# Kernel tuning notes

Measured on AMD Instinct MI355X. Metric: run time of the kernel, lower is better.

The kernel has to match this reference:

```python
import jax, jax.numpy as jnp
import numpy as np

N_NODES = 100000
N_EDGES = 1600000
D_IN = 128
D_HID = 128
D_OUT = 128


def setup_inputs() -> dict:
    key = jax.random.key(0)
    ks = jax.random.split(key, 12)
    x = jax.random.normal(ks[0], (N_NODES, D_IN), dtype=jnp.float32)
    edge_index = jax.random.randint(ks[1], (2, N_EDGES), 0, N_NODES, dtype=jnp.int64)
    s = 0.05
    # GraphConv layer l: out = agg @ w_rel + x @ w_root + b  (lin_rel has bias, lin_root does not)
    w_rel1 = jax.random.normal(ks[2], (D_IN, D_HID), dtype=jnp.float32) * s
    w_root1 = jax.random.normal(ks[3], (D_IN, D_HID), dtype=jnp.float32) * s
    b1 = jax.random.normal(ks[4], (D_HID,), dtype=jnp.float32) * s
    w_rel2 = jax.random.normal(ks[5], (D_HID, D_HID), dtype=jnp.float32) * s
    w_root2 = jax.random.normal(ks[6], (D_HID, D_HID), dtype=jnp.float32) * s
    b2 = jax.random.normal(ks[7], (D_HID,), dtype=jnp.float32) * s
    w_rel3 = jax.random.normal(ks[8], (D_HID, D_OUT), dtype=jnp.float32) * s
    w_root3 = jax.random.normal(ks[9], (D_HID, D_OUT), dtype=jnp.float32) * s
    b3 = jax.random.normal(ks[10], (D_OUT,), dtype=jnp.float32) * s
    return {"x": x, "edge_index": edge_index,
            "w_rel1": w_rel1, "w_root1": w_root1, "b1": b1,
            "w_rel2": w_rel2, "w_root2": w_root2, "b2": b2,
            "w_rel3": w_rel3, "w_root3": w_root3, "b3": b3}


def _graph_conv(h, src, dst, w_rel, w_root, b):
    # sum-aggregate neighbor features (message = x_j, flow src -> dst),
    # then linear; identical math to PyG GraphConv with aggr='add'.
    agg = jax.ops.segment_sum(h[src], dst, num_segments=h.shape[0])
    return agg @ w_rel + h @ w_root + b


def reference(x, edge_index, w_rel1, w_root1, b1, w_rel2, w_root2, b2, w_rel3, w_root3, b3):
    src, dst = edge_index[0], edge_index[1]
    h = jax.nn.relu(_graph_conv(x, src, dst, w_rel1, w_root1, b1))
    h = jax.nn.relu(_graph_conv(h, src, dst, w_rel2, w_root2, b2))
    out = _graph_conv(h, src, dst, w_rel3, w_root3, b3)
    return out
```

## Files before the change

### kernel.cpp

```cpp
#include <hip/hip_runtime.h>
#include <hip/hip_bf16.h>
#include <stdint.h>

typedef __hip_bfloat16 bf16;
typedef __hip_bfloat162 bf162;

typedef __attribute__((ext_vector_type(8))) short short8;
typedef __attribute__((ext_vector_type(4))) float floatx4;

#define BSH   8
#define BSZ   256
#define CHUNK 8192
#define NBMAX 512
#define NSLAB 8



__device__ __forceinline__ void acc2(float& a, float& b, unsigned u) {
    a += __uint_as_float(u << 16);
    b += __uint_as_float(u & 0xffff0000u);
}

__global__ __launch_bounds__(256)
void prep_bhist_kernel(const float* __restrict__ x, bf16* __restrict__ y, int n4, int nCvt,
                       const float* __restrict__ wr1, const float* __restrict__ wo1,
                       const float* __restrict__ wr2, const float* __restrict__ wo2,
                       const float* __restrict__ wr3, const float* __restrict__ wo3,
                       bf16* __restrict__ w1, bf16* __restrict__ w2, bf16* __restrict__ w3,
                       const int* __restrict__ dst, int* __restrict__ T,
                       int E, int NB, int GB) {
    __shared__ int lh[NBMAX];
    const int b = blockIdx.x;
    if (b < nCvt) {
        const int i = b * 256 + threadIdx.x;
        if (i < n4) {
            const int N = n4 >> 5;
            const int n = i >> 5;
            const int q = i & 31;
            float4 v = ((const float4*)x)[i];
            union { bf16 bb[4]; unsigned long long u; } pk;
            pk.bb[0] = __float2bfloat16(v.x);
            pk.bb[1] = __float2bfloat16(v.y);
            pk.bb[2] = __float2bfloat16(v.z);
            pk.bb[3] = __float2bfloat16(v.w);
            *(unsigned long long*)(y + ((size_t)(q >> 2) * N + n) * 16 + (q & 3) * 4) = pk.u;
        }
        return;
    }
    if (b < nCvt + 48) {
        int t = (b - nCvt) * 256 + threadIdx.x;
        const int layer = t >> 12;
        t &= 4095;
        const float* wrel  = (layer == 0) ? wr1 : (layer == 1) ? wr2 : wr3;
        const float* wroot = (layer == 0) ? wo1 : (layer == 1) ? wo2 : wo3;
        bf16*        wsw   = (layer == 0) ? w1  : (layer == 1) ? w2  : w3;
        const int lane = t & 63;
        const int ct   = (t >> 6) & 7;
        const int kt   = t >> 9;
        const int kbase = kt * 32 + (lane >> 4) * 8;
        const int n     = ct * 16 + (lane & 15);
        bf16* q = wsw + (size_t)t * 8;
#pragma unroll
        for (int j = 0; j < 8; ++j) {
            const int k = kbase + j;
            const float v = (k < 128) ? wrel[k * 128 + n] : wroot[(k - 128) * 128 + n];
            q[j] = __float2bfloat16(v);
        }
        return;
    }
    const int bb = b - nCvt - 48;
    for (int u = threadIdx.x; u < NB; u += 256) lh[u] = 0;
    __syncthreads();
    const int beg = bb * CHUNK, end = min(beg + CHUNK, E);
    for (int e = beg + threadIdx.x; e < end; e += 256)
        atomicAdd(&lh[dst[e] >> BSH], 1);
    __syncthreads();
    for (int u = threadIdx.x; u < NB; u += 256)
        T[u * GB + bb] = lh[u];
}


__global__ __launch_bounds__(256)
void scan1_kernel(const int* __restrict__ deg, int* __restrict__ rp,
                  int* __restrict__ bsum, int n) {
    __shared__ int s[256];
    const int tid = threadIdx.x;
    const int i = blockIdx.x * 256 + tid;
    const int d = (i < n) ? deg[i] : 0;
    s[tid] = d;
    __syncthreads();
    for (int off = 1; off < 256; off <<= 1) {
        int u = (tid >= off) ? s[tid - off] : 0;
        __syncthreads();
        s[tid] += u;
        __syncthreads();
    }
    if (i < n) rp[i] = s[tid] - d;
    if (tid == 255) bsum[blockIdx.x] = s[255];
}

__global__ __launch_bounds__(512)
void scan2_kernel(int* __restrict__ bsum, int G) {
    __shared__ int s[512];
    const int tid = threadIdx.x;
    const int d = (tid < G) ? bsum[tid] : 0;
    s[tid] = d;
    __syncthreads();
    for (int off = 1; off < 512; off <<= 1) {
        int u = (tid >= off) ? s[tid - off] : 0;
        __syncthreads();
        s[tid] += u;
        __syncthreads();
    }
    if (tid < G) bsum[tid] = s[tid] - d;
}


__global__ __launch_bounds__(256)
void bscatter_kernel(const int* __restrict__ src, const int* __restrict__ dst,
                     const int* __restrict__ T, const int* __restrict__ bsum,
                     int* __restrict__ ebuf, int E, int NB, int GB) {
    __shared__ int lofs[NBMAX];
    const int b = blockIdx.x;
    for (int u = threadIdx.x; u < NB; u += 256) {
        const int idx = u * GB + b;
        lofs[u] = T[idx] + bsum[idx >> 8];
    }
    __syncthreads();
    const int beg = b * CHUNK, end = min(beg + CHUNK, E);
    for (int e = beg + threadIdx.x; e < end; e += 256) {
        const int d = dst[e];
        const int u = d >> BSH;
        const int pos = atomicAdd(&lofs[u], 1);
        ebuf[pos] = (src[e] << BSH) | (d & (BSZ - 1));
    }
}

__global__ __launch_bounds__(256)
void bbuild_kernel(const int* __restrict__ T, const int* __restrict__ bsum,
                   const int* __restrict__ ebuf,
                   int* __restrict__ rp, int* __restrict__ col,
                   int E, int N, int NB, int GB) {
    __shared__ int s[256];
    __shared__ int lrank[256];
    const int u = blockIdx.x;
    const int tid = threadIdx.x;
    const int i0 = u * GB;
    const int beg = T[i0] + bsum[i0 >> 8];
    const int i1 = (u + 1) * GB;
    const int end = (u + 1 < NB) ? (T[i1] + bsum[i1 >> 8]) : E;

    lrank[tid] = 0;
    __syncthreads();
    for (int e = beg + tid; e < end; e += 256)
        atomicAdd(&lrank[ebuf[e] & (BSZ - 1)], 1);
    __syncthreads();
    const int cntv = lrank[tid];
    s[tid] = cntv;
    __syncthreads();
    for (int off = 1; off < 256; off <<= 1) {
        int v = (tid >= off) ? s[tid - off] : 0;
        __syncthreads();
        s[tid] += v;
        __syncthreads();
    }
    const int excl = s[tid] - cntv;
    const int node = u * BSZ + tid;
    if (node < N) rp[node] = beg + excl;
    if (u == NB - 1 && tid == 0) rp[N] = E;
    lrank[tid] = beg + excl;
    __syncthreads();
    for (int e = beg + tid; e < end; e += 256) {
        const int p = ebuf[e];
        const int pos = atomicAdd(&lrank[p & (BSZ - 1)], 1);
        col[pos] = p >> BSH;
    }
}


__global__ __launch_bounds__(512)
void agg_kernel(const bf16* __restrict__ h, const int* __restrict__ rp,
                const int* __restrict__ col, bf16* __restrict__ agg, int N) {
    const int s    = blockIdx.x & 7;
    const int tid  = threadIdx.x;
    const int wid  = tid >> 6;
    const int lane = tid & 63;
    const int g    = lane >> 2;
    const int fl   = lane & 3;
    const int node = (blockIdx.x >> 3) * 128 + wid * 16 + g;
    if (node >= N) return;

    const bf16* Hs = h + (size_t)s * N * 16;
    const int beg = rp[node], end = rp[node + 1];

    float a0 = 0.f, a1 = 0.f, a2 = 0.f, a3 = 0.f;
    int e = beg;
#pragma unroll 2
    for (; e + 2 <= end; e += 2) {
        const int s0 = col[e];
        const int s1 = col[e + 1];
        const uint2 r0 = *(const uint2*)(Hs + (size_t)s0 * 16 + fl * 4);
        const uint2 r1 = *(const uint2*)(Hs + (size_t)s1 * 16 + fl * 4);
        acc2(a0, a1, r0.x); acc2(a2, a3, r0.y);
        acc2(a0, a1, r1.x); acc2(a2, a3, r1.y);
    }
    if (e < end) {
        const int s0 = col[e];
        const uint2 r0 = *(const uint2*)(Hs + (size_t)s0 * 16 + fl * 4);
        acc2(a0, a1, r0.x); acc2(a2, a3, r0.y);
    }

    union { bf16 bb[4]; unsigned long long u; } pk;
    pk.bb[0] = __float2bfloat16(a0);
    pk.bb[1] = __float2bfloat16(a1);
    pk.bb[2] = __float2bfloat16(a2);
    pk.bb[3] = __float2bfloat16(a3);
    __builtin_nontemporal_store(pk.u,
        (unsigned long long*)(agg + ((size_t)s * N + node) * 16 + fl * 4));
}


template <bool RELU, typename OT>
__global__ __launch_bounds__(512)
void mfma_gemm_kernel(const bf16* __restrict__ Aagg, const bf16* __restrict__ Hroot,
                      const bf16* __restrict__ wsw, const float* __restrict__ bias,
                      OT* __restrict__ out, int M) {
    __shared__ __align__(16) char smem[67584];
    const int tid = threadIdx.x;

#pragma unroll
    for (int i = 0; i < 8; ++i) {
        const int off = i * 8192 + tid * 16;
        *(float4*)(smem + off) = *(const float4*)((const char*)wsw + off);
    }
    __syncthreads();

    const int lane = tid & 63;
    const int wave = tid >> 6;
    const int l15  = lane & 15;
    const int quad = lane >> 4;
    const int base = blockIdx.x * 128;
    const int row_a = base + wave * 16 + l15;
    const bool rowok = row_a < M;
    const bf16* wl = (const bf16*)smem;

    floatx4 acc[8];
#pragma unroll
    for (int ct = 0; ct < 8; ++ct) acc[ct] = (floatx4){0.f, 0.f, 0.f, 0.f};

#pragma unroll
    for (int kt = 0; kt < 8; ++kt) {
        const bf16* Abase = (kt < 4) ? Aagg : Hroot;
        const int k0 = (kt & 3) * 32 + quad * 8;
        short8 afrag = (short8){0, 0, 0, 0, 0, 0, 0, 0};
        if (rowok)
            afrag = *(const short8*)(Abase + ((size_t)(k0 >> 4) * M + row_a) * 16 + (k0 & 15));
#pragma unroll
        for (int ct = 0; ct < 8; ++ct) {
            const short8 bfrag = *(const short8*)(wl + (size_t)((kt * 8 + ct) * 64 + lane) * 8);
            acc[ct] = __builtin_amdgcn_mfma_f32_16x16x32_bf16(afrag, bfrag, acc[ct], 0, 0, 0);
        }
    }

    __syncthreads();
    const int rloc = wave * 16 + quad * 4;

    if constexpr (sizeof(OT) == 2) {
        bf16* tl = (bf16*)smem;
#pragma unroll
        for (int ct = 0; ct < 8; ++ct) {
            const int colc = ct * 16 + l15;
            const float bv = bias[colc];
#pragma unroll
            for (int r = 0; r < 4; ++r) {
                float v = acc[ct][r] + bv;
                if (RELU) v = fmaxf(v, 0.f);
                tl[(rloc + r) * 136 + colc] = __float2bfloat16(v);
            }
        }
        __syncthreads();
#pragma unroll
        for (int i = 0; i < 4; ++i) {
            const int chunk = i * 512 + tid;
            const int slab = chunk >> 8;
            const int r    = (chunk >> 1) & 127;
            const int half = chunk & 1;
            if (base + r < M)
                *(float4*)((char*)out + ((size_t)slab * M + base + r) * 32 + half * 16) =
                    *(const float4*)(smem + r * 272 + slab * 32 + half * 16);
        }
    } else {
        float* tl = (float*)smem;
#pragma unroll
        for (int ct = 0; ct < 8; ++ct) {
            const int colc = ct * 16 + l15;
            const float bv = bias[colc];
#pragma unroll
            for (int r = 0; r < 4; ++r) {
                float v = acc[ct][r] + bv;
                if (RELU) v = fmaxf(v, 0.f);
                tl[(rloc + r) * 132 + colc] = v;
            }
        }
        __syncthreads();
#pragma unroll
        for (int i = 0; i < 8; ++i) {
            const int chunk = i * 512 + tid;
            const int row = chunk >> 5;
            const int c   = chunk & 31;
            if (base + row < M)
                *(float4*)((char*)out + (size_t)(base + row) * 512 + c * 16) =
                    *(const float4*)(smem + row * 528 + c * 16);
        }
    }
}


extern "C" void kernel_launch(void* const* d_in, const int* in_sizes, int n_in,
                              void* d_out, int out_size, void* d_ws, size_t ws_size,
                              hipStream_t stream) {
    const float* x       = (const float*)d_in[0];
    const int*   ei      = (const int*)d_in[1];
    const float* w_rel1  = (const float*)d_in[2];
    const float* w_root1 = (const float*)d_in[3];
    const float* b1      = (const float*)d_in[4];
    const float* w_rel2  = (const float*)d_in[5];
    const float* w_root2 = (const float*)d_in[6];
    const float* b2      = (const float*)d_in[7];
    const float* w_rel3  = (const float*)d_in[8];
    const float* w_root3 = (const float*)d_in[9];
    const float* b3      = (const float*)d_in[10];
    float* out = (float*)d_out;

    const int N = in_sizes[0] / 128;
    const int E = in_sizes[1] / 2;
    const int* src = ei;
    const int* dst = ei + E;

    char* w = (char*)d_ws;
    auto alloc = [&](size_t bytes) {
        char* p = w;
        w += (bytes + 255) & ~(size_t)255;
        return p;
    };
    int*  col  = (int*)alloc((size_t)E * 4);
    int*  rp   = (int*)alloc((size_t)(N + 1) * 4);
    bf16* h1   = (bf16*)alloc((size_t)N * 128 * 2);
    bf16* xbf  = (bf16*)alloc((size_t)N * 128 * 2);
    bf16* aggb = (bf16*)alloc((size_t)N * 128 * 2);
    bf16* wsw1 = (bf16*)alloc(32768 * 2);
    bf16* wsw2 = (bf16*)alloc(32768 * 2);
    bf16* wsw3 = (bf16*)alloc(32768 * 2);
    bf16* h2   = xbf;
    int*  T    = (int*)h1;
    int*  bsum = (int*)(h1 + 1024 * 1024);
    int*  ebuf = (int*)aggb;

    const int NB = (N + BSZ - 1) / BSZ;
    const int GB = (E + CHUNK - 1) / CHUNK;
    const int nT = NB * GB;
    const int scanTBlocks = (nT + 255) / 256;

    const int aggBlocks  = 8 * ((N + 127) / 128);
    const int gemmBlocks = (N + 127) / 128;
    const int cvtBlocks  = (N * 32 + 255) / 256;

    prep_bhist_kernel<<<cvtBlocks + 48 + GB, 256, 0, stream>>>(
        x, xbf, N * 32, cvtBlocks,
        w_rel1, w_root1, w_rel2, w_root2, w_rel3, w_root3,
        wsw1, wsw2, wsw3,
        dst, T, E, NB, GB);

    scan1_kernel<<<scanTBlocks, 256, 0, stream>>>(T, T, bsum, nT);
    scan2_kernel<<<1, 512, 0, stream>>>(bsum, scanTBlocks);
    bscatter_kernel<<<GB, 256, 0, stream>>>(src, dst, T, bsum, ebuf, E, NB, GB);
    bbuild_kernel<<<NB, 256, 0, stream>>>(T, bsum, ebuf, rp, col, E, N, NB, GB);

    agg_kernel<<<aggBlocks, 512, 0, stream>>>(xbf, rp, col, aggb, N);
    mfma_gemm_kernel<true, bf16><<<gemmBlocks, 512, 0, stream>>>(aggb, xbf, wsw1, b1, h1, N);
    agg_kernel<<<aggBlocks, 512, 0, stream>>>(h1, rp, col, aggb, N);
    mfma_gemm_kernel<true, bf16><<<gemmBlocks, 512, 0, stream>>>(aggb, h1, wsw2, b2, h2, N);
    agg_kernel<<<aggBlocks, 512, 0, stream>>>(h2, rp, col, aggb, N);
    mfma_gemm_kernel<false, float><<<gemmBlocks, 512, 0, stream>>>(aggb, h2, wsw3, b3, out, N);
}
```

Before: 479.3 us.

## Parallelize aggregation over edges within a wavefront with shuffle reduction

The aggregation kernel now assigns each wavefront four nodes processed one at a time. The 16 lane groups of a wavefront split that node's edge list, covering 32 edges per iteration, and partial sums are combined with xor shuffles. Previously each 4-lane group walked one node's edges serially. The goal is more memory-level parallelism and less load imbalance from variable node degree, at the cost of shuffle reductions, masked tail work and wasted lanes on low-degree nodes (average degree is about 16).

```diff
diff --git a/kernel.cpp b/kernel.cpp
--- a/kernel.cpp
+++ b/kernel.cpp
@@ -13,6 +13,7 @@
 #define CHUNK 8192
 #define NBMAX 512
 #define NSLAB 8
+#define NPW   4
 
 
 
@@ -182,41 +183,59 @@
 void agg_kernel(const bf16* __restrict__ h, const int* __restrict__ rp,
                 const int* __restrict__ col, bf16* __restrict__ agg, int N) {
     const int s    = blockIdx.x & 7;
-    const int tid  = threadIdx.x;
-    const int wid  = tid >> 6;
-    const int lane = tid & 63;
-    const int g    = lane >> 2;
+    const int wid  = threadIdx.x >> 6;
+    const int lane = threadIdx.x & 63;
+    const int ep   = lane >> 2;
     const int fl   = lane & 3;
-    const int node = (blockIdx.x >> 3) * 128 + wid * 16 + g;
-    if (node >= N) return;
-
     const bf16* Hs = h + (size_t)s * N * 16;
-    const int beg = rp[node], end = rp[node + 1];
-
-    float a0 = 0.f, a1 = 0.f, a2 = 0.f, a3 = 0.f;
-    int e = beg;
-#pragma unroll 2
-    for (; e + 2 <= end; e += 2) {
-        const int s0 = col[e];
-        const int s1 = col[e + 1];
-        const uint2 r0 = *(const uint2*)(Hs + (size_t)s0 * 16 + fl * 4);
-        const uint2 r1 = *(const uint2*)(Hs + (size_t)s1 * 16 + fl * 4);
-        acc2(a0, a1, r0.x); acc2(a2, a3, r0.y);
-        acc2(a0, a1, r1.x); acc2(a2, a3, r1.y);
-    }
-    if (e < end) {
-        const int s0 = col[e];
-        const uint2 r0 = *(const uint2*)(Hs + (size_t)s0 * 16 + fl * 4);
-        acc2(a0, a1, r0.x); acc2(a2, a3, r0.y);
-    }
-
-    union { bf16 bb[4]; unsigned long long u; } pk;
-    pk.bb[0] = __float2bfloat16(a0);
-    pk.bb[1] = __float2bfloat16(a1);
-    pk.bb[2] = __float2bfloat16(a2);
-    pk.bb[3] = __float2bfloat16(a3);
-    __builtin_nontemporal_store(pk.u,
-        (unsigned long long*)(agg + ((size_t)s * N + node) * 16 + fl * 4));
+    bf16* As = agg + (size_t)s * N * 16;
+
+    const int node0 = ((blockIdx.x >> 3) * 8 + wid) * NPW;
+
+#pragma unroll 1
+    for (int ni = 0; ni < NPW; ++ni) {
+        const int node = node0 + ni;
+        if (node >= N) return;
+        const int beg = rp[node], end = rp[node + 1];
+        float a0 = 0.f, a1 = 0.f, a2 = 0.f, a3 = 0.f;
+        int e = beg;
+        for (; e + 32 <= end; e += 32) {
+            const int c0 = col[e + ep];
+            const int c1 = col[e + 16 + ep];
+            const uint2 r0 = *(const uint2*)(Hs + (size_t)c0 * 16 + fl * 4);
+            const uint2 r1 = *(const uint2*)(Hs + (size_t)c1 * 16 + fl * 4);
+            acc2(a0, a1, r0.x); acc2(a2, a3, r0.y);
+            acc2(a0, a1, r1.x); acc2(a2, a3, r1.y);
+        }
+        if (e < end) {
+            const int e0 = e + ep;
+            const int c0 = col[(e0 < end) ? e0 : (end - 1)];
+            const uint2 r0 = *(const uint2*)(Hs + (size_t)c0 * 16 + fl * 4);
+            if (e0 < end) { acc2(a0, a1, r0.x); acc2(a2, a3, r0.y); }
+            if (e + 16 < end) {
+                const int e1 = e + 16 + ep;
+                const int c1 = col[(e1 < end) ? e1 : (end - 1)];
+                const uint2 r1 = *(const uint2*)(Hs + (size_t)c1 * 16 + fl * 4);
+                if (e1 < end) { acc2(a0, a1, r1.x); acc2(a2, a3, r1.y); }
+            }
+        }
+#pragma unroll
+        for (int m = 4; m <= 32; m <<= 1) {
+            a0 += __shfl_xor(a0, m, 64);
+            a1 += __shfl_xor(a1, m, 64);
+            a2 += __shfl_xor(a2, m, 64);
+            a3 += __shfl_xor(a3, m, 64);
+        }
+        if (lane < 4) {
+            union { bf16 bb[4]; unsigned long long u; } pk;
+            pk.bb[0] = __float2bfloat16(a0);
+            pk.bb[1] = __float2bfloat16(a1);
+            pk.bb[2] = __float2bfloat16(a2);
+            pk.bb[3] = __float2bfloat16(a3);
+            __builtin_nontemporal_store(pk.u,
+                (unsigned long long*)(As + (size_t)node * 16 + lane * 4));
+        }
+    }
 }
 
 
@@ -361,7 +380,8 @@
     const int nT = NB * GB;
     const int scanTBlocks = (nT + 255) / 256;
 
-    const int aggBlocks  = 8 * ((N + 127) / 128);
+    const int nodesPerBlk = 8 * NPW;
+    const int aggBlocks  = 8 * ((N + nodesPerBlk - 1) / nodesPerBlk);
     const int gemmBlocks = (N + 127) / 128;
     const int cvtBlocks  = (N * 32 + 255) / 256;
 
```

After: 746.9 us. 1.56x slower.
